# Performance work log

Hardware: AMD Instinct MI355X
Metric: run time of the kernel (lower is better)

Reference implementation:

```python
import jax, jax.numpy as jnp
import numpy as np

H_DIM = 1152
N_HEADS = 12
HEAD_DIM = H_DIM // N_HEADS  # 96, divisible by 3
SCALE_ROT = 32 // 16  # character_pixel_size // patch_size


def setup_inputs() -> dict:
    key = jax.random.key(0)
    ks = jax.random.split(key, 9)
    std = 1.0 / np.sqrt(H_DIM)
    return {
        "hidden_states": jax.random.normal(ks[0], (8, 1025, H_DIM), dtype=jnp.float32),
        "Wq": jax.random.normal(ks[1], (H_DIM, H_DIM), dtype=jnp.float32) * std,
        "bq": jax.random.normal(ks[2], (H_DIM,), dtype=jnp.float32) * 0.02,
        "Wk": jax.random.normal(ks[3], (H_DIM, H_DIM), dtype=jnp.float32) * std,
        "bk": jax.random.normal(ks[4], (H_DIM,), dtype=jnp.float32) * 0.02,
        "Wv": jax.random.normal(ks[5], (H_DIM, H_DIM), dtype=jnp.float32) * std,
        "bv": jax.random.normal(ks[6], (H_DIM,), dtype=jnp.float32) * 0.02,
        "Wo": jax.random.normal(ks[7], (H_DIM, H_DIM), dtype=jnp.float32) * std,
        "bo": jax.random.normal(ks[8], (H_DIM,), dtype=jnp.float32) * 0.02,
        "rows": 32,
        "cols": 32,
    }


def _rotary_tables(seq_len, rows, cols, dtype):
    # (seq_len, n_triplets) trig tables based on 2-D patch grid position
    inv_freq = 1.0 / (10000.0 ** (jnp.arange(0, HEAD_DIM, 3, dtype=dtype) / (HEAD_DIM * SCALE_ROT)))
    ids = jnp.arange(seq_len)
    cls_offset = 1 if seq_len != rows * cols else 0
    grid_ids = jnp.clip(ids - cls_offset, 0)
    row_ids = (grid_ids // cols).astype(dtype)
    col_ids = (grid_ids % cols).astype(dtype)
    theta = row_ids[:, None] * inv_freq
    psi = col_ids[:, None] * inv_freq
    return jnp.cos(theta), jnp.sin(theta), jnp.cos(psi), jnp.sin(psi)


def _apply_rotary_3d(x, ct, st, cp, sp):
    # x: (b, s, h, d) -> view as (b, s, h, t, 3)
    b, s, h, d = x.shape
    x = x.reshape(b, s, h, d // 3, 3)
    ct = ct[None, :, None, :]
    st = st[None, :, None, :]
    cp = cp[None, :, None, :]
    sp = sp[None, :, None, :]
    x0, x1, x2 = x[..., 0], x[..., 1], x[..., 2]
    r0 = cp * x0 + sp * st * x1 + sp * ct * x2
    r1 = ct * x1 - st * x2
    r2 = -sp * x0 + cp * st * x1 + cp * ct * x2
    return jnp.stack((r0, r1, r2), axis=-1).reshape(b, s, h, d)


def reference(hidden_states, Wq, bq, Wk, bk, Wv, bv, Wo, bo, rows, cols):
    b, s, _ = hidden_states.shape
    dtype = hidden_states.dtype
    scale = HEAD_DIM ** -0.5

    q = (hidden_states @ Wq + bq).reshape(b, s, N_HEADS, HEAD_DIM)
    k = (hidden_states @ Wk + bk).reshape(b, s, N_HEADS, HEAD_DIM)
    v = (hidden_states @ Wv + bv).reshape(b, s, N_HEADS, HEAD_DIM)

    ct, st, cp, sp = _rotary_tables(s, rows, cols, dtype)
    q = _apply_rotary_3d(q, ct, st, cp, sp)
    k = _apply_rotary_3d(k, ct, st, cp, sp)

    # (b, h, s, s) attention scores
    scores = jnp.einsum("bqhd,bkhd->bhqk", q, k) * scale
    probs = jax.nn.softmax(scores.astype(jnp.float32), axis=-1).astype(dtype)
    ctx = jnp.einsum("bhqk,bkhd->bqhd", probs, v).reshape(b, s, H_DIM)
    out = ctx @ Wo + bo
    return out
```

## Files before the change

### kernel.cpp

```cpp
#include <hip/hip_runtime.h>
#include <stdint.h>

#define BATCH 8
#define SEQ   1025
#define HDIM  1152
#define NH    12
#define DH    96
#define MROWS (BATCH*SEQ)
#define N_QKV (3*HDIM)
#define KD    HDIM
#define NTK   36

typedef __attribute__((ext_vector_type(8))) short short8;
typedef __attribute__((ext_vector_type(4))) short short4_;
typedef __attribute__((ext_vector_type(4))) float float4_;
typedef __attribute__((ext_vector_type(16))) float f32x16;

#define AS1 __attribute__((address_space(1)))
#define AS3 __attribute__((address_space(3)))
#define BARM() do { asm volatile("" ::: "memory"); __builtin_amdgcn_s_barrier(); asm volatile("" ::: "memory"); } while (0)

__device__ inline float bf2f(short s) {
  union { unsigned u; float f; } x; x.u = ((unsigned)(unsigned short)s) << 16; return x.f;
}
__device__ inline short f2bf(float f) {
  union { float f; unsigned u; } x; x.f = f;
  unsigned r = (x.u + 0x7fffu + ((x.u >> 16) & 1u)) >> 16;
  return (short)r;
}

__global__ __launch_bounds__(256) void convx(const float* __restrict__ hs, short* __restrict__ X) {
  int i = blockIdx.x * 256 + threadIdx.x;
  float4_ v = ((const float4_*)hs)[i];
  short4_ o;
  o[0] = f2bf(v[0]); o[1] = f2bf(v[1]); o[2] = f2bf(v[2]); o[3] = f2bf(v[3]);
  ((short4_*)X)[i] = o;
}

__global__ __launch_bounds__(256) void convw_t(const float* __restrict__ W0,
                                               const float* __restrict__ W1,
                                               const float* __restrict__ W2,
                                               short* __restrict__ Wt) {
  __shared__ float T[64][65];
  const int z = blockIdx.z;
  const float* W = z == 0 ? W0 : (z == 1 ? W1 : W2);
  const int n0 = blockIdx.x * 64, k0 = blockIdx.y * 64;
  const int tid = threadIdx.x;
  const int r = tid >> 2, cq = (tid & 3) * 16;
#pragma unroll
  for (int u = 0; u < 4; ++u) {
    float4_ v = *(const float4_*)&W[(long)(k0 + r) * HDIM + n0 + cq + u * 4];
    T[r][cq + u * 4 + 0] = v[0]; T[r][cq + u * 4 + 1] = v[1];
    T[r][cq + u * 4 + 2] = v[2]; T[r][cq + u * 4 + 3] = v[3];
  }
  __syncthreads();
  const int n = tid >> 2, kq = (tid & 3) * 16;
  short out[16];
#pragma unroll
  for (int u = 0; u < 16; ++u) out[u] = f2bf(T[kq + u][n]);
  short* dst = Wt + (long)(z * HDIM + n0 + n) * KD + k0 + kq;
  *(short8*)dst = *(short8*)&out[0];
  *(short8*)(dst + 8) = *(short8*)&out[8];
}

template<int OUTF32>
__global__ __launch_bounds__(512, 1) void gemm256(
    const short* __restrict__ A, const short* __restrict__ Bt,
    const float* __restrict__ b0, const float* __restrict__ b1, const float* __restrict__ b2,
    void* __restrict__ Cout, const int N, const int MT) {
  __shared__ alignas(16) short Lds[49152];
  const int tid = threadIdx.x;
  const int l = tid & 63, w = tid >> 6;
  const int lrow = l & 15, lg = l >> 4;
  const int wr = w >> 2, wc = w & 3;

  const int nwg = gridDim.x;
  const int qq = nwg >> 3, r8 = nwg & 7;
  const int xcd = blockIdx.x & 7, loc = blockIdx.x >> 3;
  const int wg = (xcd < r8 ? xcd * (qq + 1) : r8 * (qq + 1) + (xcd - r8) * qq) + loc;
  const int mt = wg % MT, nt = wg / MT;
  const int m0 = mt * 256, n0 = nt * 256;

  const short* asrc[2]; const short* bsrc[2];
#pragma unroll
  for (int i = 0; i < 2; ++i) {
    int p = i * 512 + tid;
    int wl = (p & 7) ^ ((p >> 3) & 7);
    int row = ((p >> 3) << 1) | (wl >> 2);
    int kc = (wl & 3) * 8;
    int ra = m0 + row; if (ra > MROWS - 1) ra = MROWS - 1;
    int rb = n0 + row; if (rb > N - 1) rb = N - 1;
    asrc[i] = A + (long)ra * KD + kc;
    bsrc[i] = Bt + (long)rb * KD + kc;
  }

#define STAGEA(bi, kt_, i) \
  __builtin_amdgcn_global_load_lds((const AS1 void*)(asrc[i] + (kt_) * 32), \
      (AS3 void*)(&Lds[(bi) * 8192 + (i * 512 + tid) * 8]), 16, 0, 0)
#define STAGEB(bi, kt_, i) \
  __builtin_amdgcn_global_load_lds((const AS1 void*)(bsrc[i] + (kt_) * 32), \
      (AS3 void*)(&Lds[24576 + (bi) * 8192 + (i * 512 + tid) * 8]), 16, 0, 0)
#define LDA(dst, abase, mi) { const int row_ = wr * 128 + (mi) * 16 + lrow; \
  dst = *(const short8*)&Lds[(abase) + ((row_ >> 1) << 6) + \
      (((((row_ & 1) << 2) + lg) ^ ((row_ >> 1) & 7)) << 3)]; }
#define LDB(dst, bbase, nj) { const int row_ = wc * 64 + (nj) * 16 + lrow; \
  dst = *(const short8*)&Lds[(bbase) + ((row_ >> 1) << 6) + \
      (((((row_ & 1) << 2) + lg) ^ ((row_ >> 1) & 7)) << 3)]; }
#define MFMA16(a, b, c) __builtin_amdgcn_mfma_f32_16x16x32_bf16(a, b, c, 0, 0, 0)

  float4_ acc[8][4];
#pragma unroll
  for (int mi = 0; mi < 8; ++mi)
#pragma unroll
    for (int nj = 0; nj < 4; ++nj) acc[mi][nj] = (float4_)(0.f);

  STAGEA(0, 0, 0); STAGEA(0, 0, 1); STAGEB(0, 0, 0); STAGEB(0, 0, 1);
  STAGEA(1, 1, 0); STAGEA(1, 1, 1); STAGEB(1, 1, 0); STAGEB(1, 1, 1);
  asm volatile("s_waitcnt vmcnt(4)" ::: "memory");
  BARM();

  int cur = 0, st = 2;
  for (int kt = 0; kt < NTK; ++kt) {
    const bool dost = (kt + 2) < NTK;
    const int abase = cur * 8192, bbase = 24576 + cur * 8192;
    short8 a0, a1, a2, a3, bb0, bb1, bb2, bb3;
    LDA(a0, abase, 0); LDA(a1, abase, 1); LDA(a2, abase, 2); LDA(a3, abase, 3);
    LDB(bb0, bbase, 0); LDB(bb1, bbase, 1); LDB(bb2, bbase, 2); LDB(bb3, bbase, 3);
    if (dost) { STAGEA(st, kt + 2, 0); STAGEA(st, kt + 2, 1); }
    BARM();
    asm volatile("s_waitcnt lgkmcnt(0)" ::: "memory");
    __builtin_amdgcn_sched_barrier(0);
    __builtin_amdgcn_s_setprio(1);
    acc[0][0] = MFMA16(a0, bb0, acc[0][0]);
    acc[0][1] = MFMA16(a0, bb1, acc[0][1]);
    acc[0][2] = MFMA16(a0, bb2, acc[0][2]);
    acc[0][3] = MFMA16(a0, bb3, acc[0][3]);
    acc[1][0] = MFMA16(a1, bb0, acc[1][0]);
    acc[1][1] = MFMA16(a1, bb1, acc[1][1]);
    acc[1][2] = MFMA16(a1, bb2, acc[1][2]);
    acc[1][3] = MFMA16(a1, bb3, acc[1][3]);
    acc[2][0] = MFMA16(a2, bb0, acc[2][0]);
    acc[2][1] = MFMA16(a2, bb1, acc[2][1]);
    acc[2][2] = MFMA16(a2, bb2, acc[2][2]);
    acc[2][3] = MFMA16(a2, bb3, acc[2][3]);
    acc[3][0] = MFMA16(a3, bb0, acc[3][0]);
    acc[3][1] = MFMA16(a3, bb1, acc[3][1]);
    acc[3][2] = MFMA16(a3, bb2, acc[3][2]);
    acc[3][3] = MFMA16(a3, bb3, acc[3][3]);
    __builtin_amdgcn_s_setprio(0);
    BARM();
    LDA(a0, abase, 4); LDA(a1, abase, 5); LDA(a2, abase, 6); LDA(a3, abase, 7);
    if (dost) {
      STAGEB(st, kt + 2, 0); STAGEB(st, kt + 2, 1);
      asm volatile("s_waitcnt vmcnt(4)" ::: "memory");
    } else if (kt + 1 < NTK) {
      asm volatile("s_waitcnt vmcnt(0)" ::: "memory");
    }
    BARM();
    asm volatile("s_waitcnt lgkmcnt(0)" ::: "memory");
    __builtin_amdgcn_sched_barrier(0);
    __builtin_amdgcn_s_setprio(1);
    acc[4][0] = MFMA16(a0, bb0, acc[4][0]);
    acc[4][1] = MFMA16(a0, bb1, acc[4][1]);
    acc[4][2] = MFMA16(a0, bb2, acc[4][2]);
    acc[4][3] = MFMA16(a0, bb3, acc[4][3]);
    acc[5][0] = MFMA16(a1, bb0, acc[5][0]);
    acc[5][1] = MFMA16(a1, bb1, acc[5][1]);
    acc[5][2] = MFMA16(a1, bb2, acc[5][2]);
    acc[5][3] = MFMA16(a1, bb3, acc[5][3]);
    acc[6][0] = MFMA16(a2, bb0, acc[6][0]);
    acc[6][1] = MFMA16(a2, bb1, acc[6][1]);
    acc[6][2] = MFMA16(a2, bb2, acc[6][2]);
    acc[6][3] = MFMA16(a2, bb3, acc[6][3]);
    acc[7][0] = MFMA16(a3, bb0, acc[7][0]);
    acc[7][1] = MFMA16(a3, bb1, acc[7][1]);
    acc[7][2] = MFMA16(a3, bb2, acc[7][2]);
    acc[7][3] = MFMA16(a3, bb3, acc[7][3]);
    __builtin_amdgcn_s_setprio(0);
    BARM();
    cur = cur == 2 ? 0 : cur + 1;
    st = st == 2 ? 0 : st + 1;
  }

  float bias[4];
#pragma unroll
  for (int nj = 0; nj < 4; ++nj) {
    int cn = n0 + wc * 64 + nj * 16 + lrow;
    float bv_ = 0.f;
    if (cn < N) bv_ = (N == HDIM) ? b0[cn]
                                  : (cn < HDIM ? b0[cn] : (cn < 2 * HDIM ? b1[cn - HDIM] : b2[cn - 2 * HDIM]));
    bias[nj] = bv_;
  }
#pragma unroll
  for (int mi = 0; mi < 8; ++mi)
#pragma unroll
    for (int r = 0; r < 4; ++r) {
      int m = m0 + wr * 128 + mi * 16 + lg * 4 + r;
      if (m >= MROWS) continue;
#pragma unroll
      for (int nj = 0; nj < 4; ++nj) {
        int cn = n0 + wc * 64 + nj * 16 + lrow;
        if (cn >= N) continue;
        float v = acc[mi][nj][r] + bias[nj];
        if (OUTF32) ((float*)Cout)[(long)m * N + cn] = v;
        else        ((short*)Cout)[(long)m * N + cn] = f2bf(v);
      }
    }
#undef STAGEA
#undef STAGEB
#undef LDA
#undef LDB
#undef MFMA16
}

__global__ __launch_bounds__(256) void rotary_q(short* __restrict__ QKV,
                                                const int* __restrict__ rowsp,
                                                const int* __restrict__ colsp) {
  int idx = blockIdx.x * 256 + threadIdx.x;
  if (idx >= MROWS * NH * 4) return;
  const int qt = idx & 3;
  const int hm = idx >> 2;
  const int h = hm % NH, m = hm / NH;
  const int s = m % SEQ;
  const int cols = colsp[0], rws = rowsp[0];
  const int off = (SEQ != rws * cols) ? 1 : 0;
  int gid = s - off; if (gid < 0) gid = 0;
  const float frow = (float)(gid / cols), fcol = (float)(gid % cols);
  union { short sh[24]; short8 v[3]; } u;
  short* p = QKV + (long)m * N_QKV + h * DH + qt * 24;
  u.v[0] = *(short8*)p; u.v[1] = *(short8*)(p + 8); u.v[2] = *(short8*)(p + 16);
#pragma unroll
  for (int t = 0; t < 8; ++t) {
    int j = qt * 8 + t;
    float invf = exp2f((float)(3 * j) * (-13.287712379549449f / 192.0f));
    float st, ct, sp, cp;
    __sincosf(frow * invf, &st, &ct);
    __sincosf(fcol * invf, &sp, &cp);
    float x0 = bf2f(u.sh[3 * t]), x1 = bf2f(u.sh[3 * t + 1]), x2 = bf2f(u.sh[3 * t + 2]);
    u.sh[3 * t]     = f2bf( cp * x0 + sp * st * x1 + sp * ct * x2);
    u.sh[3 * t + 1] = f2bf( ct * x1 - st * x2);
    u.sh[3 * t + 2] = f2bf(-sp * x0 + cp * st * x1 + cp * ct * x2);
  }
  *(short8*)p = u.v[0]; *(short8*)(p + 8) = u.v[1]; *(short8*)(p + 16) = u.v[2];
}

__global__ __launch_bounds__(256) void fragpack(const short* __restrict__ QKV,
                                                short* __restrict__ Kf,
                                                short* __restrict__ Vf,
                                                const int* __restrict__ rowsp,
                                                const int* __restrict__ colsp) {
  __shared__ short L[64 * 96];
  const int t = blockIdx.x, bh = blockIdx.y;
  const int b = bh / NH, h = bh % NH;
  const int tid = threadIdx.x;
#pragma unroll
  for (int i = 0; i < 3; ++i) {
    int cc = i * 256 + tid;
    int kv = cc / 384;
    int rm = cc % 384;
    int r = rm / 12, m = rm % 12;
    int s = t * 32 + r; if (s > SEQ - 1) s = SEQ - 1;
    const short* src = QKV + (long)(b * SEQ + s) * N_QKV + (kv ? 2 * HDIM : HDIM) + h * DH + m * 8;
    *(short8*)&L[cc * 8] = *(const short8*)src;
  }
  __syncthreads();
  {
    const int cols = colsp[0], rws = rowsp[0];
    const int off = (SEQ != rws * cols) ? 1 : 0;
#pragma unroll
    for (int i = 0; i < 4; ++i) {
      int idx2 = i * 256 + tid;
      int r = idx2 >> 5, j = idx2 & 31;
      int s = t * 32 + r; if (s > SEQ - 1) s = SEQ - 1;
      int gid = s - off; if (gid < 0) gid = 0;
      float invf = exp2f((float)(3 * j) * (-13.287712379549449f / 192.0f));
      float st, ct, sp, cp;
      __sincosf((float)(gid / cols) * invf, &st, &ct);
      __sincosf((float)(gid % cols) * invf, &sp, &cp);
      short* pp = &L[r * 96 + 3 * j];
      float x0 = bf2f(pp[0]), x1 = bf2f(pp[1]), x2 = bf2f(pp[2]);
      pp[0] = f2bf( cp * x0 + sp * st * x1 + sp * ct * x2);
      pp[1] = f2bf( ct * x1 - st * x2);
      pp[2] = f2bf(-sp * x0 + cp * st * x1 + cp * ct * x2);
    }
  }
  __syncthreads();
#pragma unroll
  for (int i = 0; i < 3; ++i) {
    int oc = i * 256 + tid;
    if (oc < 384) {
      int c = oc / 64, ll = oc & 63;
      int qi = ll & 31, hi = ll >> 5;
      short8 v = *(const short8*)&L[qi * 96 + c * 16 + hi * 8];
      *(short8*)(Kf + (((long)(bh * 33 + t) * 6 + c) * 64 + ll) * 8) = v;
    } else {
      int oc2 = oc - 384;
      int d = oc2 / 128, sl = (oc2 / 64) & 1, ll = oc2 & 63;
      int qi = ll & 31, hi = ll >> 5;
      short8 v;
#pragma unroll
      for (int j = 0; j < 8; ++j)
        v[j] = L[32 * 96 + (sl * 16 + hi * 8 + j) * 96 + d * 32 + qi];
      *(short8*)(Vf + ((((long)(bh * 33 + t) * 3 + d) * 2 + sl) * 64 + ll) * 8) = v;
    }
  }
}

__global__ __launch_bounds__(128, 3) void attn_kernel(const short* __restrict__ QKV,
                                                      const short* __restrict__ Kf,
                                                      const short* __restrict__ Vf,
                                                      short* __restrict__ CTX) {
  const int tid = threadIdx.x;
  const int l = tid & 63, w = tid >> 6;
  const int qi = l & 31, hi = l >> 5;
  const int bid = blockIdx.x;
  const int xcd = bid & 7, jj = bid >> 3;
  const int bh = xcd * 12 + jj / 17;
  const int qb = jj % 17;
  const int b = bh / NH, h = bh % NH;
  const int s = qb * 64 + w * 32 + qi;
  const int sq = s > SEQ - 1 ? SEQ - 1 : s;

  const float scale = 0.1020620726159658f;
  const short* Qr = QKV + (long)(b * SEQ + sq) * N_QKV + h * DH;
  short8 qf[6];
#pragma unroll
  for (int c = 0; c < 6; ++c) {
    short8 v = *(const short8*)(Qr + c * 16 + hi * 8);
#pragma unroll
    for (int j = 0; j < 8; ++j) v[j] = f2bf(bf2f(v[j]) * scale);
    qf[c] = v;
  }

  const short* Kb = Kf + (long)bh * 33 * 6 * 64 * 8;
  const short* Vb = Vf + (long)bh * 33 * 6 * 64 * 8;

  f32x16 ctxv[3];
#pragma unroll
  for (int d = 0; d < 3; ++d) ctxv[d] = (f32x16)(0.f);
  float m_ = -1e30f, l_ = 0.f;

  for (int t = 0; t < 33; ++t) {
    f32x16 S = (f32x16)(0.f);
#pragma unroll
    for (int c = 0; c < 6; ++c) {
      short8 kf = *(const short8*)(Kb + (((long)t * 6 + c) * 64 + l) * 8);
      S = __builtin_amdgcn_mfma_f32_32x32x16_bf16(kf, qf[c], S, 0, 0, 0);
    }
    if (t == 32) {
      S[0] = hi ? -1e30f : S[0];
#pragma unroll
      for (int r = 1; r < 16; ++r) S[r] = -1e30f;
    }
    float tm = S[0];
#pragma unroll
    for (int r = 1; r < 16; ++r) tm = fmaxf(tm, S[r]);
    tm = fmaxf(tm, __shfl_xor(tm, 32));
    if (!__all(tm - m_ <= 8.f)) {
      float mn = fmaxf(m_, tm);
      float alpha = __expf(m_ - mn);
      m_ = mn;
      l_ *= alpha;
#pragma unroll
      for (int d = 0; d < 3; ++d)
#pragma unroll
        for (int r = 0; r < 16; ++r) ctxv[d][r] *= alpha;
    }
    float ts = 0.f;
#pragma unroll
    for (int r = 0; r < 16; ++r) { float p = __expf(S[r] - m_); S[r] = p; ts += p; }
    ts += __shfl_xor(ts, 32);
    l_ += ts;

    unsigned pk_[8];
#pragma unroll
    for (int j = 0; j < 8; ++j)
      pk_[j] = (unsigned)(unsigned short)f2bf(S[2 * j]) |
               ((unsigned)(unsigned short)f2bf(S[2 * j + 1]) << 16);
    unsigned s0 = hi ? pk_[0] : pk_[2];
    unsigned s1 = hi ? pk_[1] : pk_[3];
    unsigned s2 = hi ? pk_[4] : pk_[6];
    unsigned s3 = hi ? pk_[5] : pk_[7];
    unsigned r0 = __shfl_xor(s0, 32);
    unsigned r1 = __shfl_xor(s1, 32);
    unsigned r2 = __shfl_xor(s2, 32);
    unsigned r3 = __shfl_xor(s3, 32);
    union PF { unsigned u[4]; short8 s8; } f0, f1;
    f0.u[0] = hi ? r0 : pk_[0];
    f0.u[1] = hi ? r1 : pk_[1];
    f0.u[2] = hi ? pk_[2] : r0;
    f0.u[3] = hi ? pk_[3] : r1;
    f1.u[0] = hi ? r2 : pk_[4];
    f1.u[1] = hi ? r3 : pk_[5];
    f1.u[2] = hi ? pk_[6] : r2;
    f1.u[3] = hi ? pk_[7] : r3;

#pragma unroll
    for (int d = 0; d < 3; ++d) {
      const short* Vr = Vb + (((long)t * 3 + d) * 2 * 64) * 8;
      short8 vf0 = *(const short8*)(Vr + l * 8);
      ctxv[d] = __builtin_amdgcn_mfma_f32_32x32x16_bf16(vf0, f0.s8, ctxv[d], 0, 0, 0);
      short8 vf1 = *(const short8*)(Vr + (64 + l) * 8);
      ctxv[d] = __builtin_amdgcn_mfma_f32_32x32x16_bf16(vf1, f1.s8, ctxv[d], 0, 0, 0);
    }
  }

  float invl = 1.f / l_;
  if (s <= SEQ - 1) {
    short* Cr = CTX + (long)(b * SEQ + s) * HDIM + h * DH;
#pragma unroll
    for (int d = 0; d < 3; ++d)
#pragma unroll
      for (int g = 0; g < 4; ++g) {
        short4_ o;
#pragma unroll
        for (int r = 0; r < 4; ++r) o[r] = f2bf(ctxv[d][4 * g + r] * invl);
        *(short4_*)(Cr + d * 32 + 8 * g + 4 * hi) = o;
      }
  }
}

extern "C" void kernel_launch(void* const* d_in, const int* in_sizes, int n_in,
                              void* d_out, int out_size, void* d_ws, size_t ws_size,
                              hipStream_t stream) {
  const float* hs = (const float*)d_in[0];
  const float* Wq = (const float*)d_in[1];
  const float* bq = (const float*)d_in[2];
  const float* Wk = (const float*)d_in[3];
  const float* bk = (const float*)d_in[4];
  const float* Wv = (const float*)d_in[5];
  const float* bv = (const float*)d_in[6];
  const float* Wo = (const float*)d_in[7];
  const float* bo = (const float*)d_in[8];
  const int* rows = (const int*)d_in[9];
  const int* cols = (const int*)d_in[10];
  float* out = (float*)d_out;

  char* ws = (char*)d_ws;
  short* X   = (short*)(ws);
  short* Wt  = (short*)(ws + 18892800);
  short* Wot = (short*)(ws + 26855424);
  short* QKV = (short*)(ws + 29509632);
  short* Vf  = (short*)(ws + 86188032);
  short* CTX = (short*)(ws + 105652224);
  short* Kf  = (short*)(ws);

  convx<<<9225, 256, 0, stream>>>(hs, X);
  convw_t<<<dim3(18, 18, 3), 256, 0, stream>>>(Wq, Wk, Wv, Wt);
  convw_t<<<dim3(18, 18, 1), 256, 0, stream>>>(Wo, Wo, Wo, Wot);
  gemm256<0><<<462, 512, 0, stream>>>(X, Wt, bq, bk, bv, QKV, N_QKV, 33);
  rotary_q<<<1538, 256, 0, stream>>>(QKV, rows, cols);
  fragpack<<<dim3(33, 96), 256, 0, stream>>>(QKV, Kf, Vf, rows, cols);
  attn_kernel<<<1632, 128, 0, stream>>>(QKV, Kf, Vf, CTX);
  gemm256<1><<<165, 512, 0, stream>>>(CTX, Wot, bo, bo, bo, out, HDIM, 33);
}
```

Before: 280.3 us.

## Shrink GEMM tiles to 128x128 with 256 threads and multiple blocks per CU

The projection GEMM kernel moves from 256x256 tiles with 512 threads and one block per CU to 128x128 tiles with 256 threads and up to three resident blocks per CU. The K-loop is simplified to a single MFMA phase per step, with all next-stage loads issued up front and one barrier per iteration. Grids grow accordingly (1755 and 585 blocks), which improves wave quantization on the small output GEMM and lets co-resident blocks hide latency. The trade-off is lower operand reuse per tile, so global and LDS traffic per FLOP rises, and the setprio/sched_barrier scheduling hints are dropped.

New measurement: 287.2 us. 1.02x slower.

```diff
diff --git a/kernel.cpp b/kernel.cpp
--- a/kernel.cpp
+++ b/kernel.cpp
@@ -64,27 +64,27 @@
 }
 
 template<int OUTF32>
-__global__ __launch_bounds__(512, 1) void gemm256(
+__global__ __launch_bounds__(256, 3) void gemm256(
     const short* __restrict__ A, const short* __restrict__ Bt,
     const float* __restrict__ b0, const float* __restrict__ b1, const float* __restrict__ b2,
     void* __restrict__ Cout, const int N, const int MT) {
-  __shared__ alignas(16) short Lds[49152];
+  __shared__ alignas(16) short Lds[24576];
   const int tid = threadIdx.x;
   const int l = tid & 63, w = tid >> 6;
   const int lrow = l & 15, lg = l >> 4;
-  const int wr = w >> 2, wc = w & 3;
+  const int wr = w >> 1, wc = w & 1;
 
   const int nwg = gridDim.x;
   const int qq = nwg >> 3, r8 = nwg & 7;
   const int xcd = blockIdx.x & 7, loc = blockIdx.x >> 3;
   const int wg = (xcd < r8 ? xcd * (qq + 1) : r8 * (qq + 1) + (xcd - r8) * qq) + loc;
   const int mt = wg % MT, nt = wg / MT;
-  const int m0 = mt * 256, n0 = nt * 256;
+  const int m0 = mt * 128, n0 = nt * 128;
 
   const short* asrc[2]; const short* bsrc[2];
 #pragma unroll
   for (int i = 0; i < 2; ++i) {
-    int p = i * 512 + tid;
+    int p = i * 256 + tid;
     int wl = (p & 7) ^ ((p >> 3) & 7);
     int row = ((p >> 3) << 1) | (wl >> 2);
     int kc = (wl & 3) * 8;
@@ -96,11 +96,11 @@
 
 #define STAGEA(bi, kt_, i) \
   __builtin_amdgcn_global_load_lds((const AS1 void*)(asrc[i] + (kt_) * 32), \
-      (AS3 void*)(&Lds[(bi) * 8192 + (i * 512 + tid) * 8]), 16, 0, 0)
+      (AS3 void*)(&Lds[(bi) * 4096 + (i * 256 + tid) * 8]), 16, 0, 0)
 #define STAGEB(bi, kt_, i) \
   __builtin_amdgcn_global_load_lds((const AS1 void*)(bsrc[i] + (kt_) * 32), \
-      (AS3 void*)(&Lds[24576 + (bi) * 8192 + (i * 512 + tid) * 8]), 16, 0, 0)
-#define LDA(dst, abase, mi) { const int row_ = wr * 128 + (mi) * 16 + lrow; \
+      (AS3 void*)(&Lds[12288 + (bi) * 4096 + (i * 256 + tid) * 8]), 16, 0, 0)
+#define LDA(dst, abase, mi) { const int row_ = wr * 64 + (mi) * 16 + lrow; \
   dst = *(const short8*)&Lds[(abase) + ((row_ >> 1) << 6) + \
       (((((row_ & 1) << 2) + lg) ^ ((row_ >> 1) & 7)) << 3)]; }
 #define LDB(dst, bbase, nj) { const int row_ = wc * 64 + (nj) * 16 + lrow; \
@@ -108,9 +108,9 @@
       (((((row_ & 1) << 2) + lg) ^ ((row_ >> 1) & 7)) << 3)]; }
 #define MFMA16(a, b, c) __builtin_amdgcn_mfma_f32_16x16x32_bf16(a, b, c, 0, 0, 0)
 
-  float4_ acc[8][4];
-#pragma unroll
-  for (int mi = 0; mi < 8; ++mi)
+  float4_ acc[4][4];
+#pragma unroll
+  for (int mi = 0; mi < 4; ++mi)
 #pragma unroll
     for (int nj = 0; nj < 4; ++nj) acc[mi][nj] = (float4_)(0.f);
 
@@ -119,18 +119,17 @@
   asm volatile("s_waitcnt vmcnt(4)" ::: "memory");
   BARM();
 
-  int cur = 0, st = 2;
   for (int kt = 0; kt < NTK; ++kt) {
+    const int cur = kt % 3, st = (kt + 2) % 3;
     const bool dost = (kt + 2) < NTK;
-    const int abase = cur * 8192, bbase = 24576 + cur * 8192;
+    const int abase = cur * 4096, bbase = 12288 + cur * 4096;
+    if (dost) {
+      STAGEA(st, kt + 2, 0); STAGEA(st, kt + 2, 1);
+      STAGEB(st, kt + 2, 0); STAGEB(st, kt + 2, 1);
+    }
     short8 a0, a1, a2, a3, bb0, bb1, bb2, bb3;
+    LDB(bb0, bbase, 0); LDB(bb1, bbase, 1); LDB(bb2, bbase, 2); LDB(bb3, bbase, 3);
     LDA(a0, abase, 0); LDA(a1, abase, 1); LDA(a2, abase, 2); LDA(a3, abase, 3);
-    LDB(bb0, bbase, 0); LDB(bb1, bbase, 1); LDB(bb2, bbase, 2); LDB(bb3, bbase, 3);
-    if (dost) { STAGEA(st, kt + 2, 0); STAGEA(st, kt + 2, 1); }
-    BARM();
-    asm volatile("s_waitcnt lgkmcnt(0)" ::: "memory");
-    __builtin_amdgcn_sched_barrier(0);
-    __builtin_amdgcn_s_setprio(1);
     acc[0][0] = MFMA16(a0, bb0, acc[0][0]);
     acc[0][1] = MFMA16(a0, bb1, acc[0][1]);
     acc[0][2] = MFMA16(a0, bb2, acc[0][2]);
@@ -147,39 +146,10 @@
     acc[3][1] = MFMA16(a3, bb1, acc[3][1]);
     acc[3][2] = MFMA16(a3, bb2, acc[3][2]);
     acc[3][3] = MFMA16(a3, bb3, acc[3][3]);
-    __builtin_amdgcn_s_setprio(0);
+    if (dost)                asm volatile("s_waitcnt vmcnt(4)" ::: "memory");
+    else if (kt == NTK - 2)  asm volatile("s_waitcnt vmcnt(0)" ::: "memory");
+    asm volatile("s_waitcnt lgkmcnt(0)" ::: "memory");
     BARM();
-    LDA(a0, abase, 4); LDA(a1, abase, 5); LDA(a2, abase, 6); LDA(a3, abase, 7);
-    if (dost) {
-      STAGEB(st, kt + 2, 0); STAGEB(st, kt + 2, 1);
-      asm volatile("s_waitcnt vmcnt(4)" ::: "memory");
-    } else if (kt + 1 < NTK) {
-      asm volatile("s_waitcnt vmcnt(0)" ::: "memory");
-    }
-    BARM();
-    asm volatile("s_waitcnt lgkmcnt(0)" ::: "memory");
-    __builtin_amdgcn_sched_barrier(0);
-    __builtin_amdgcn_s_setprio(1);
-    acc[4][0] = MFMA16(a0, bb0, acc[4][0]);
-    acc[4][1] = MFMA16(a0, bb1, acc[4][1]);
-    acc[4][2] = MFMA16(a0, bb2, acc[4][2]);
-    acc[4][3] = MFMA16(a0, bb3, acc[4][3]);
-    acc[5][0] = MFMA16(a1, bb0, acc[5][0]);
-    acc[5][1] = MFMA16(a1, bb1, acc[5][1]);
-    acc[5][2] = MFMA16(a1, bb2, acc[5][2]);
-    acc[5][3] = MFMA16(a1, bb3, acc[5][3]);
-    acc[6][0] = MFMA16(a2, bb0, acc[6][0]);
-    acc[6][1] = MFMA16(a2, bb1, acc[6][1]);
-    acc[6][2] = MFMA16(a2, bb2, acc[6][2]);
-    acc[6][3] = MFMA16(a2, bb3, acc[6][3]);
-    acc[7][0] = MFMA16(a3, bb0, acc[7][0]);
-    acc[7][1] = MFMA16(a3, bb1, acc[7][1]);
-    acc[7][2] = MFMA16(a3, bb2, acc[7][2]);
-    acc[7][3] = MFMA16(a3, bb3, acc[7][3]);
-    __builtin_amdgcn_s_setprio(0);
-    BARM();
-    cur = cur == 2 ? 0 : cur + 1;
-    st = st == 2 ? 0 : st + 1;
   }
 
   float bias[4];
@@ -192,10 +162,10 @@
     bias[nj] = bv_;
   }
 #pragma unroll
-  for (int mi = 0; mi < 8; ++mi)
+  for (int mi = 0; mi < 4; ++mi)
 #pragma unroll
     for (int r = 0; r < 4; ++r) {
-      int m = m0 + wr * 128 + mi * 16 + lg * 4 + r;
+      int m = m0 + wr * 64 + mi * 16 + lg * 4 + r;
       if (m >= MROWS) continue;
 #pragma unroll
       for (int nj = 0; nj < 4; ++nj) {
@@ -448,9 +418,9 @@
   convx<<<9225, 256, 0, stream>>>(hs, X);
   convw_t<<<dim3(18, 18, 3), 256, 0, stream>>>(Wq, Wk, Wv, Wt);
   convw_t<<<dim3(18, 18, 1), 256, 0, stream>>>(Wo, Wo, Wo, Wot);
-  gemm256<0><<<462, 512, 0, stream>>>(X, Wt, bq, bk, bv, QKV, N_QKV, 33);
+  gemm256<0><<<1755, 256, 0, stream>>>(X, Wt, bq, bk, bv, QKV, N_QKV, 65);
   rotary_q<<<1538, 256, 0, stream>>>(QKV, rows, cols);
   fragpack<<<dim3(33, 96), 256, 0, stream>>>(QKV, Kf, Vf, rows, cols);
   attn_kernel<<<1632, 128, 0, stream>>>(QKV, Kf, Vf, CTX);
-  gemm256<1><<<165, 512, 0, stream>>>(CTX, Wot, bo, bo, bo, out, HDIM, 33);
-}
+  gemm256<1><<<585, 256, 0, stream>>>(CTX, Wot, bo, bo, bo, out, HDIM, 65);
+}
```
